# Kernel tuning notes

Measured on AMD Instinct MI355X. Metric: run time of the kernel, lower is better.

Reference implementation:

```python
import jax, jax.numpy as jnp
import numpy as np

B, C, H, W = 64, 2048, 14, 14
D, S, ITERS, EPS, HID = 256, 8, 3, 1e-8, 512


def build_pos(h, w, d):
    gy, gx = np.meshgrid(np.arange(h), np.arange(w), indexing='ij')
    q = d // 4
    omega = 1.0 / (10000.0 ** (np.arange(q) / q))
    ey = gy.reshape(-1, 1) * omega
    ex = gx.reshape(-1, 1) * omega
    pe = np.concatenate([np.sin(ey), np.cos(ey), np.sin(ex), np.cos(ex)], axis=1)
    return jnp.asarray(pe[None], jnp.float32)  # (1, h*w, d)


def layernorm(x, g, b, eps=1e-5):
    m = x.mean(-1, keepdims=True)
    v = ((x - m) ** 2).mean(-1, keepdims=True)
    return (x - m) * jax.lax.rsqrt(v + eps) * g + b


def setup_inputs() -> dict:
    key = jax.random.key(0)
    ks = jax.random.split(key, 16)
    w = lambda k, shp, s=0.02: jax.random.normal(k, shp, jnp.float32) * s
    inp = {
        'x': jax.random.normal(ks[0], (B, C, H, W), jnp.float32),
        'slot_noise': jax.random.normal(ks[1], (B, S, D), jnp.float32),
        'conv_w': w(ks[2], (C, D)), 'conv_b': jnp.zeros((D,), jnp.float32),
        'pos': build_pos(H, W, D),
        'slots_mu': jax.random.normal(ks[3], (1, 1, D), jnp.float32),
        'slots_logsigma': -jnp.ones((1, 1, D), jnp.float32),
        'qw': w(ks[4], (D, D)), 'qb': jnp.zeros((D,), jnp.float32),
        'kw': w(ks[5], (D, D)), 'kb': jnp.zeros((D,), jnp.float32),
        'vw': w(ks[6], (D, D)), 'vb': jnp.zeros((D,), jnp.float32),
        'gru_wih': w(ks[7], (D, 3 * D)), 'gru_whh': w(ks[8], (D, 3 * D)),
        'gru_bih': jnp.zeros((3 * D,), jnp.float32), 'gru_bhh': jnp.zeros((3 * D,), jnp.float32),
        'w1': w(ks[9], (D, HID)), 'b1': jnp.zeros((HID,), jnp.float32),
        'w2': w(ks[10], (HID, D)), 'b2': jnp.zeros((D,), jnp.float32),
        'ln_in_g': jnp.ones((D,), jnp.float32), 'ln_in_b': jnp.zeros((D,), jnp.float32),
        'ln_s_g': jnp.ones((D,), jnp.float32), 'ln_s_b': jnp.zeros((D,), jnp.float32),
        'ln_ff_g': jnp.ones((D,), jnp.float32), 'ln_ff_b': jnp.zeros((D,), jnp.float32),
    }
    return inp


def reference(x, slot_noise, conv_w, conv_b, pos, slots_mu, slots_logsigma,
              qw, qb, kw, kb, vw, vb, gru_wih, gru_whh, gru_bih, gru_bhh,
              w1, b1, w2, b2, ln_in_g, ln_in_b, ln_s_g, ln_s_b, ln_ff_g, ln_ff_b):
    b, c, h, w_ = x.shape
    d = qw.shape[0]
    scale = d ** (-0.5)
    # (B,C,H,W) -> (B,N,C) -> project -> add pos
    xt = x.transpose(0, 2, 3, 1).reshape(b, h * w_, c)
    xt = xt @ conv_w + conv_b + pos
    # slot init
    slots = slots_mu + jnp.exp(slots_logsigma) * slot_noise  # (B,S,D)
    inp = layernorm(xt, ln_in_g, ln_in_b)
    k = inp @ kw + kb
    v = inp @ vw + vb
    attn = None
    for _ in range(ITERS):
        slots_prev = slots
        s = layernorm(slots, ln_s_g, ln_s_b)
        q = s @ qw + qb
        dots = jnp.einsum('bid,bjd->bij', q, k) * scale  # (B,S,N)
        attn = jax.nn.softmax(dots, axis=1) + EPS  # softmax over slots
        attn = attn / attn.sum(-1, keepdims=True)  # renormalize over keys
        updates = jnp.einsum('bjd,bij->bid', v, attn)  # (B,S,D)
        # GRUCell (torch semantics)
        gi = updates @ gru_wih + gru_bih
        gh = slots_prev @ gru_whh + gru_bhh
        ir, iz, inn = jnp.split(gi, 3, axis=-1)
        hr, hz, hn = jnp.split(gh, 3, axis=-1)
        r = jax.nn.sigmoid(ir + hr)
        z = jax.nn.sigmoid(iz + hz)
        nn_ = jnp.tanh(inn + r * hn)
        slots = (1.0 - z) * nn_ + z * slots_prev
        ff = layernorm(slots, ln_ff_g, ln_ff_b)
        slots = slots + (jax.nn.relu(ff @ w1 + b1)) @ w2 + b2
    attn_map = attn.reshape(b, S, h, w_)
    return slots, attn_map
```

## Files before the change

kernel.cpp:

```cpp
#include <hip/hip_runtime.h>
#include <stdint.h>

#define HWN 196
#define CIN 2048
#define DD  256
#define BB  64
#define NSLOT 8
#define KVPAD 224
#define MTOT 12544
#define BKP 128

typedef __attribute__((ext_vector_type(8))) short short8;
typedef __attribute__((ext_vector_type(4))) float f32x4;
typedef __attribute__((ext_vector_type(4))) unsigned short us4;

__device__ __forceinline__ ushort f2bf(float f){ union{float f;uint32_t u;}v;v.f=f;uint32_t u=v.u;return (ushort)((u+0x7FFFu+((u>>16)&1u))>>16);}
__device__ __forceinline__ float bf2f(ushort h){ union{uint32_t u;float f;}v;v.u=((uint32_t)h)<<16;return v.f;}
__device__ __forceinline__ float sigm(float x){ return 1.f/(1.f+expf(-x)); }

__device__ __forceinline__ short8 ldsY(const ushort* buf, int LD, int kt, int lane){
    int row = lane & 15;
    int ch = kt*4 + (lane>>4);
    return *(const short8*)&buf[row*LD + ((ch ^ (row&7))<<3)];
}
// ... 49 lines not shown
        #pragma unroll
        for (int j = 0; j < 8; ++j){ av0[j] = (short)f2bf(areg[j]); av1[j] = (short)f2bf(areg[8+j]); }
        int ch0 = kg*2;
        *(short8*)&As[0][am*BKP + ((ch0^(am&7))<<3)] = av0;
        *(short8*)&As[0][am*BKP + (((ch0+1)^(am&7))<<3)] = av1;
    }
    __syncthreads();
    int cur = 0;
    for (int kt = 0; kt < 8; ++kt){
        if (kt < 7){
            #pragma unroll
            for (int j = 0; j < 16; ++j)
                areg[j] = aptr[(size_t)((kt+1)*BKP + kg*16+j)*HWN];
        }
        short8 bfr[4][2];
        #pragma unroll
        for (int kk = 0; kk < 4; ++kk)
            #pragma unroll
            for (int ni = 0; ni < 2; ++ni){
                int n = wv*32 + ni*16 + (lane&15);
                bfr[kk][ni] = *(const short8*)&cwT[(size_t)n*CIN + kbase + kt*BKP + kk*32 + (lane>>4)*8];
            }
        #pragma unroll
        for (int kk = 0; kk < 4; ++kk){
            short8 afr[4];
            #pragma unroll
            for (int mi = 0; mi < 4; ++mi){
                int row = mi*16 + (lane&15);
                int ch = kk*4 + (lane>>4);
                afr[mi] = *(const short8*)&As[cur][row*BKP + ((ch^(row&7))<<3)];
            }
            #pragma unroll
            for (int mi = 0; mi < 4; ++mi)
                #pragma unroll
                for (int ni = 0; ni < 2; ++ni)
                    acc[mi][ni] = __builtin_amdgcn_mfma_f32_16x16x32_bf16(afr[mi], bfr[kk][ni], acc[mi][ni], 0,0,0);
        }
        if (kt < 7){
            short8 av0, av1;
            #pragma unroll
            for (int j = 0; j < 8; ++j){ av0[j] = (short)f2bf(areg[j]); av1[j] = (short)f2bf(areg[8+j]); }
            int ch0 = kg*2;
            *(short8*)&As[cur^1][am*BKP + ((ch0^(am&7))<<3)] = av0;
            *(short8*)&As[cur^1][am*BKP + (((ch0+1)^(am&7))<<3)] = av1;
        }
        __syncthreads();
        cur ^= 1;
    }
    float* outp = Cpart + (size_t)kq*MTOT*DD;
    #pragma unroll
    for (int mi = 0; mi < 4; ++mi){
        #pragma unroll
        for (int ni = 0; ni < 2; ++ni){
            int n = wv*32 + ni*16 + (lane&15);
            #pragma unroll
            for (int r = 0; r < 4; ++r){
                int m = bm + mi*16 + (lane>>4)*4 + r;
                outp[(size_t)m*DD + n] = acc[mi][ni][r];
            }
        }
    }
}

__global__ __launch_bounds__(512) void k_red(const float* __restrict__ Cpart,
        const float* __restrict__ cb, const float* __restrict__ pos,
        const float* __restrict__ lng, const float* __restrict__ lnb,
        const ushort* __restrict__ kwT, const ushort* __restrict__ vwT,
        const float* __restrict__ kb, const float* __restrict__ vb,
        ushort* __restrict__ kbf, ushort* __restrict__ vT){
    __shared__ ushort As[32*256];
    const int t = threadIdx.x, lane = t & 63, wv = t >> 6;
    const int b = blockIdx.x / 7, pblk = blockIdx.x % 7;
    {
        int row = t >> 4, seg = t & 15;
        int pin = pblk*32 + row;
        int grow = b*HWN + pin;
        if (grow > MTOT-1) grow = MTOT-1;
        int p = pin < HWN ? pin : HWN-1;
        const float* c0 = Cpart + (size_t)grow*DD + seg*16;
        const float* c1 = Cpart + (size_t)MTOT*DD + (size_t)grow*DD + seg*16;
        const float* pp = pos + (size_t)p*DD + seg*16;
        float f[16];
        float s = 0.f, sq = 0.f;
        #pragma unroll
        for (int q = 0; q < 4; ++q){
            f32x4 a  = *(const f32x4*)&c0[q*4];
            f32x4 bq = *(const f32x4*)&c1[q*4];
            f32x4 pv = *(const f32x4*)&pp[q*4];
            f32x4 cv = *(const f32x4*)&cb[seg*16 + q*4];
            #pragma unroll
            for (int r2 = 0; r2 < 4; ++r2){
                float v = a[r2] + bq[r2] + pv[r2] + cv[r2];
                f[q*4+r2] = v; s += v; sq += v*v;
            }
        }
        #pragma unroll
        for (int m = 8; m >= 1; m >>= 1){ s += __shfl_xor(s, m, 64); sq += __shfl_xor(sq, m, 64); }
        float mean = s * (1.f/256.f);
        float rs = rsqrtf(sq*(1.f/256.f) - mean*mean + 1e-5f);
        int d0 = seg*16;
        short8 o0, o1;
        #pragma unroll
        for (int j = 0; j < 8; ++j){
            o0[j] = (short)f2bf((f[j]   - mean)*rs*lng[d0+j]   + lnb[d0+j]);
            o1[j] = (short)f2bf((f[8+j] - mean)*rs*lng[d0+8+j] + lnb[d0+8+j]);
        }
        int ch0 = seg*2;
        *(short8*)&As[row*256 + ((ch0^(row&7))<<3)] = o0;
        *(short8*)&As[row*256 + (((ch0+1)^(row&7))<<3)] = o1;
    }
    __syncthreads();
    f32x4 acck[2][2] = {}, accv[2][2] = {};
    const int n0 = wv*32;
    #pragma unroll
    for (int kt = 0; kt < 8; ++kt){
        short8 afr[2];
        #pragma unroll
        for (int mi = 0; mi < 2; ++mi){
            int row = mi*16 + (lane&15);
            int ch = kt*4 + (lane>>4);
            afr[mi] = *(const short8*)&As[row*256 + ((ch^(row&7))<<3)];
        }
        #pragma unroll
        for (int ni = 0; ni < 2; ++ni){
            int n = n0 + ni*16 + (lane&15);
            int koff = kt*32 + (lane>>4)*8;
            short8 bk = *(const short8*)&kwT[(size_t)n*DD + koff];
            short8 bv = *(const short8*)&vwT[(size_t)n*DD + koff];
            #pragma unroll
            for (int mi = 0; mi < 2; ++mi){
                acck[mi][ni] = __builtin_amdgcn_mfma_f32_16x16x32_bf16(afr[mi], bk, acck[mi][ni],0,0,0);
                accv[mi][ni] = __builtin_amdgcn_mfma_f32_16x16x32_bf16(afr[mi], bv, accv[mi][ni],0,0,0);
            }
        }
    }
    #pragma unroll
    for (int mi = 0; mi < 2; ++mi){
        #pragma unroll
        for (int ni = 0; ni < 2; ++ni){
            int n = n0 + ni*16 + (lane&15);
            float kbn = kb[n], vbn = vb[n];
            int pl0 = pblk*32 + mi*16 + (lane>>4)*4;
            us4 pk;
            #pragma unroll
            for (int r = 0; r < 4; ++r){
                kbf[((size_t)b*KVPAD + pl0 + r)*DD + n] = f2bf(acck[mi][ni][r] + kbn);
                pk[r] = f2bf(accv[mi][ni][r] + vbn);
            }
            *(us4*)&vT[((size_t)b*DD + n)*KVPAD + pl0] = pk;
        }
    }
}

__global__ __launch_bounds__(512) void k_init(const float* __restrict__ noise,
        const float* __restrict__ mu, const float* __restrict__ lsig,
        const ushort* __restrict__ qwT, const float* __restrict__ qb,
        const float* __restrict__ gs, const float* __restrict__ bs,
        float* __restrict__ slots, ushort* __restrict__ qbuf){
    __shared__ float Sld[16*256];
    __shared__ ushort Ysn[16*256];
    __shared__ float part[8][16][2];
    __shared__ float stats[16][2];
    const int t = threadIdx.x, lane = t & 63, w = t >> 6;
    const int bb = blockIdx.x, rbase = bb*16;
    {
        int row = t>>5, ch = t&31; int d = ch*8;
        f32x4 n0 = *(const f32x4*)&noise[(size_t)(rbase+row)*DD + d];
        f32x4 n1 = *(const f32x4*)&noise[(size_t)(rbase+row)*DD + d + 4];
        f32x4 m0 = *(const f32x4*)&mu[d];
        f32x4 m1 = *(const f32x4*)&mu[d+4];
        f32x4 l0 = *(const f32x4*)&lsig[d];
        f32x4 l1 = *(const f32x4*)&lsig[d+4];
        f32x4 s0, s1;
        #pragma unroll
        for (int j = 0; j < 4; ++j){
            s0[j] = m0[j] + expf(l0[j])*n0[j];
            s1[j] = m1[j] + expf(l1[j])*n1[j];
        }
        *(f32x4*)&slots[(size_t)(rbase+row)*DD + d] = s0;
        *(f32x4*)&slots[(size_t)(rbase+row)*DD + d + 4] = s1;
        *(f32x4*)&Sld[row*256 + d] = s0;
        *(f32x4*)&Sld[row*256 + d + 4] = s1;
    }
    __syncthreads();
    f32x4 sv[2];
    #pragma unroll
    for (int sub = 0; sub < 2; ++sub){
        int d0 = w*32 + sub*16 + (lane>>4)*4;
        sv[sub] = *(const f32x4*)&Sld[(lane&15)*256 + d0];
    }
    {
        float lsum = 0.f, lsq = 0.f;
        #pragma unroll
        for (int sub = 0; sub < 2; ++sub)
            #pragma unroll
            for (int r = 0; r < 4; ++r){ float v = sv[sub][r]; lsum += v; lsq += v*v; }
        lsum += __shfl_xor(lsum, 16, 64); lsum += __shfl_xor(lsum, 32, 64);
        lsq  += __shfl_xor(lsq, 16, 64);  lsq  += __shfl_xor(lsq, 32, 64);
        if (lane < 16){ part[w][lane][0] = lsum; part[w][lane][1] = lsq; }
    }
    __syncthreads();
    if (t < 16){
        float a = 0.f, c = 0.f;
        #pragma unroll
        for (int i = 0; i < 8; ++i){ a += part[i][t][0]; c += part[i][t][1]; }
        float mean = a*(1.f/256.f);
        stats[t][0] = mean;
        stats[t][1] = rsqrtf(c*(1.f/256.f) - mean*mean + 1e-5f);
    }
    __syncthreads();
    {
        int slot = lane&15;
        float mean = stats[slot][0], rs = stats[slot][1];
        #pragma unroll
        for (int sub = 0; sub < 2; ++sub){
            int d0 = w*32 + sub*16 + (lane>>4)*4;
            f32x4 g4 = *(const f32x4*)&gs[d0];
            f32x4 b4 = *(const f32x4*)&bs[d0];
            us4 o;
            #pragma unroll
            for (int r = 0; r < 4; ++r) o[r] = f2bf((sv[sub][r]-mean)*rs*g4[r] + b4[r]);
            int ch = d0>>3;
            *(us4*)&Ysn[slot*256 + ((ch^(slot&7))<<3) + (d0&7)] = o;
        }
    }
    __syncthreads();
    f32x4 qa[2] = {};
    #pragma unroll
    for (int kt = 0; kt < 8; ++kt){
        short8 ysn = ldsY(Ysn, 256, kt, lane);
        #pragma unroll
        for (int sub = 0; sub < 2; ++sub){
            int nrow = w*32 + sub*16 + (lane&15);
            short8 xx = gX(qwT, 256, nrow, kt, lane);
            qa[sub] = __builtin_amdgcn_mfma_f32_16x16x32_bf16(xx, ysn, qa[sub], 0,0,0);
        }
    }
    #pragma unroll
    for (int sub = 0; sub < 2; ++sub){
        int qd0 = w*32 + sub*16 + (lane>>4)*4;
        f32x4 qb4 = *(const f32x4*)&qb[qd0];
        us4 o;
        #pragma unroll
        for (int r = 0; r < 4; ++r) o[r] = f2bf((qa[sub][r]+qb4[r])*0.0625f);
        *(us4*)&qbuf[(size_t)(rbase+(lane&15))*DD + qd0] = o;
    }
}

__global__ __launch_bounds__(512) void k_slot(
        const ushort* __restrict__ qbuf, const ushort* __restrict__ kbf,
        const ushort* __restrict__ vT, float* __restrict__ slots,
        ushort* __restrict__ qout,
        const ushort* __restrict__ wihT, const ushort* __restrict__ whhT,
        const float* __restrict__ bih, const float* __restrict__ bhh,
        const ushort* __restrict__ w1T, const float* __restrict__ b1,
        const ushort* __restrict__ w2T, const float* __restrict__ b2,
        const float* __restrict__ gff, const float* __restrict__ bff,
        const float* __restrict__ gs, const float* __restrict__ bs,
        const ushort* __restrict__ qwT, const float* __restrict__ qb,
        float* __restrict__ out_slots, float* __restrict__ out_attn,
        int final_){
    __shared__ ushort Yq[16*256];
    __shared__ ushort Xat[16*256];
    __shared__ ushort Yupd[16*256];
    __shared__ ushort Yslb[16*256];
    __shared__ ushort Ysn[16*256];
    __shared__ ushort Yh[16*512];
    __shared__ float wpart[8][16];
    __shared__ float invk[16];
    __shared__ float part[8][16][2];
    __shared__ float stats[16][2];
    const int t = threadIdx.x, lane = t & 63, w = t >> 6;
    const int b = blockIdx.x;
    const int rbase = b * NSLOT;
    const int srow = lane & 15;
    const int srd = (srow < NSLOT) ? srow : 0;

    if (t < 256){
        int row = t>>5, ch = t&31;
        short8 v = *(const short8*)&qbuf[(size_t)(rbase+row)*DD + ch*8];
        *(short8*)&Yq[row*256 + ((ch^(row&7))<<3)] = v;
        f32x4 s0 = *(const f32x4*)&slots[(size_t)(rbase+row)*DD + ch*8];
        f32x4 s1 = *(const f32x4*)&slots[(size_t)(rbase+row)*DD + ch*8 + 4];
        short8 sv;
        #pragma unroll
        for (int j = 0; j < 4; ++j){ sv[j] = (short)f2bf(s0[j]); sv[4+j] = (short)f2bf(s1[j]); }
        *(short8*)&Yslb[row*256 + ((ch^(row&7))<<3)] = sv;
    } else {
        int i = t - 256;
        int row = (i>>5) + 8, ch = i&31;
        short8 z;
        #pragma unroll
        for (int j = 0; j < 8; ++j) z[j] = 0;
        *(short8*)&Yq[row*256 + ((ch^(row&7))<<3)] = z;
        *(short8*)&Yupd[row*256 + ((ch^(row&7))<<3)] = z;
        *(short8*)&Yslb[row*256 + ((ch^(row&7))<<3)] = z;
    }
    __syncthreads();
    {
        short8 yf[8];
        #pragma unroll
        for (int kt = 0; kt < 8; ++kt) yf[kt] = ldsY(Yq, 256, kt, lane);
        float ps = 0.f;
        #pragma unroll
        for (int rep = 0; rep < 2; ++rep){
            int f = w + rep*8;
            if (f < 14){
                f32x4 acc = {};
                #pragma unroll
                for (int kt = 0; kt < 8; ++kt){
                    short8 xx = gX(kbf + (size_t)b*KVPAD*DD, 256, f*16 + (lane&15), kt, lane);
                    acc = __builtin_amdgcn_mfma_f32_16x16x32_bf16(xx, yf[kt], acc, 0,0,0);
                }
                int k0 = f*16 + (lane>>4)*4;
                us4 o;
                #pragma unroll
                for (int r = 0; r < 4; ++r){
                    float v = acc[r];
                    float mx = v;
                    mx = fmaxf(mx, __shfl_xor(mx, 1, 64));
                    mx = fmaxf(mx, __shfl_xor(mx, 2, 64));
                    mx = fmaxf(mx, __shfl_xor(mx, 4, 64));
                    float e = expf(v - mx);
                    float se = e;
                    se += __shfl_xor(se, 1, 64);
                    se += __shfl_xor(se, 2, 64);
                    se += __shfl_xor(se, 4, 64);
                    float val = e/se + 1e-8f;
                    if (k0 + r >= HWN) val = 0.f;
                    ps += val;
                    o[r] = f2bf(val);
                }
                int ch = k0 >> 3;
                *(us4*)&Xat[srow*256 + ((ch^(srow&7))<<3) + (k0&7)] = o;
            }
        }
        ps += __shfl_xor(ps, 16, 64);
        ps += __shfl_xor(ps, 32, 64);
        if (lane < 16) wpart[w][lane] = ps;
    }
    __syncthreads();
    if (t < 16){
        float s = 0.f;
        #pragma unroll
        for (int i = 0; i < 8; ++i) s += wpart[i][t];
        invk[t] = 1.f/s;
    }
    __syncthreads();
    {
        short8 xa[7];
        #pragma unroll
        for (int kt = 0; kt < 7; ++kt) xa[kt] = ldsY(Xat, 256, kt, lane);
        f32x4 iv = *(const f32x4*)&invk[(lane>>4)*4];
        #pragma unroll
        for (int i = 0; i < 2; ++i){
            int d0 = (w*2 + i)*16;
            f32x4 acc = {};
            #pragma unroll
            for (int kt = 0; kt < 7; ++kt){
                short8 y = gX(vT + (size_t)b*DD*KVPAD, KVPAD, d0 + (lane&15), kt, lane);
                acc = __builtin_amdgcn_mfma_f32_16x16x32_bf16(xa[kt], y, acc, 0,0,0);
            }
            #pragma unroll
            for (int r = 0; r < 4; ++r){
                int s2 = (lane>>4)*4 + r;
                if (s2 < NSLOT){
                    int d = d0 + (lane&15);
                    int ch = d >> 3;
                    Yupd[s2*256 + ((ch^(s2&7))<<3) + (d&7)] = f2bf(acc[r]*iv[r]);
                }
            }
        }
    }
    if (final_){
        for (int idx = t; idx < NSLOT*HWN; idx += 512){
            int slot = idx/HWN, key = idx - slot*HWN;
            int ch = key >> 3;
            out_attn[(size_t)b*NSLOT*HWN + idx] =
                bf2f(Xat[slot*256 + ((ch^(slot&7))<<3) + (key&7)]) * invk[slot];
        }
    }
    __syncthreads();
    f32x4 gi[6] = {}, gh[6] = {};
    #pragma unroll
    for (int kt = 0; kt < 8; ++kt){
        short8 yu = ldsY(Yupd, 256, kt, lane);
        short8 ys = ldsY(Yslb, 256, kt, lane);
        #pragma unroll
        for (int g = 0; g < 3; ++g)
            #pragma unroll
            for (int sub = 0; sub < 2; ++sub){
                int nrow = g*256 + w*32 + sub*16 + (lane&15);
                short8 xi = gX(wihT, 256, nrow, kt, lane);
                short8 xh = gX(whhT, 256, nrow, kt, lane);
                gi[g*2+sub] = __builtin_amdgcn_mfma_f32_16x16x32_bf16(xi, yu, gi[g*2+sub], 0,0,0);
                gh[g*2+sub] = __builtin_amdgcn_mfma_f32_16x16x32_bf16(xh, ys, gh[g*2+sub], 0,0,0);
            }
    }
    f32x4 snew[2];
    #pragma unroll
    for (int sub = 0; sub < 2; ++sub){
        int d0 = w*32 + sub*16 + (lane>>4)*4;
        f32x4 sp  = *(const f32x4*)&slots[(size_t)(rbase + srd)*DD + d0];
        f32x4 bir = *(const f32x4*)&bih[d0];
        f32x4 biz = *(const f32x4*)&bih[256 + d0];
        f32x4 bin = *(const f32x4*)&bih[512 + d0];
        f32x4 bhr = *(const f32x4*)&bhh[d0];
        f32x4 bhz = *(const f32x4*)&bhh[256 + d0];
        f32x4 bhn = *(const f32x4*)&bhh[512 + d0];
        #pragma unroll
        for (int r = 0; r < 4; ++r){
            float ir = gi[0+sub][r] + bir[r];
            float iz = gi[2+sub][r] + biz[r];
            float in_ = gi[4+sub][r] + bin[r];
            float hr = gh[0+sub][r] + bhr[r];
            float hz = gh[2+sub][r] + bhz[r];
            float hn = gh[4+sub][r] + bhn[r];
            float rr = sigm(ir + hr);
            float zz = sigm(iz + hz);
            float nn = tanhf(in_ + rr*hn);
            snew[sub][r] = (1.f - zz)*nn + zz*sp[r];
        }
    }
    {
        float lsum = 0.f, lsq = 0.f;
        #pragma unroll
        for (int sub = 0; sub < 2; ++sub)
            #pragma unroll
            for (int r = 0; r < 4; ++r){ float v = snew[sub][r]; lsum += v; lsq += v*v; }
        lsum += __shfl_xor(lsum, 16, 64); lsum += __shfl_xor(lsum, 32, 64);
        lsq  += __shfl_xor(lsq, 16, 64);  lsq  += __shfl_xor(lsq, 32, 64);
        if (lane < 16){ part[w][lane][0] = lsum; part[w][lane][1] = lsq; }
    }
    __syncthreads();
    if (t < 16){
        float a = 0.f, c = 0.f;
        #pragma unroll
        for (int i = 0; i < 8; ++i){ a += part[i][t][0]; c += part[i][t][1]; }
        float mean = a*(1.f/256.f);
        stats[t][0] = mean;
        stats[t][1] = rsqrtf(c*(1.f/256.f) - mean*mean + 1e-5f);
    }
    __syncthreads();
    {
        float mean = stats[srow][0], rs = stats[srow][1];
        #pragma unroll
        for (int sub = 0; sub < 2; ++sub){
            int d0 = w*32 + sub*16 + (lane>>4)*4;
            f32x4 g4 = *(const f32x4*)&gff[d0];
            f32x4 b4 = *(const f32x4*)&bff[d0];
            us4 o;
            #pragma unroll
            for (int r = 0; r < 4; ++r) o[r] = f2bf((snew[sub][r]-mean)*rs*g4[r] + b4[r]);
            int ch = d0 >> 3;
            *(us4*)&Ysn[srow*256 + ((ch^(srow&7))<<3) + (d0&7)] = o;
        }
    }
    __syncthreads();
    {
        f32x4 hh[4] = {};
        #pragma unroll
        for (int kt = 0; kt < 8; ++kt){
            short8 ysn = ldsY(Ysn, 256, kt, lane);
            #pragma unroll
            for (int s2 = 0; s2 < 4; ++s2){
                int nrow = w*64 + s2*16 + (lane&15);
                short8 xx = gX(w1T, 256, nrow, kt, lane);
                hh[s2] = __builtin_amdgcn_mfma_f32_16x16x32_bf16(xx, ysn, hh[s2], 0,0,0);
            }
        }
        #pragma unroll
        for (int s2 = 0; s2 < 4; ++s2){
            int n0 = w*64 + s2*16 + (lane>>4)*4;
            f32x4 b14 = *(const f32x4*)&b1[n0];
            us4 o;
            #pragma unroll
            for (int r = 0; r < 4; ++r) o[r] = f2bf(fmaxf(hh[s2][r] + b14[r], 0.f));
            int ch = n0 >> 3;
            *(us4*)&Yh[srow*512 + ((ch^(srow&7))<<3) + (n0&7)] = o;
        }
    }
    __syncthreads();
    f32x4 ns[2];
    {
        f32x4 o2[2] = {};
        #pragma unroll
        for (int kt = 0; kt < 16; ++kt){
            short8 yh = ldsY(Yh, 512, kt, lane);
            #pragma unroll
            for (int sub = 0; sub < 2; ++sub){
                int nrow = w*32 + sub*16 + (lane&15);
                short8 xx = gX(w2T, 512, nrow, kt, lane);
                o2[sub] = __builtin_amdgcn_mfma_f32_16x16x32_bf16(xx, yh, o2[sub], 0,0,0);
            }
        }
        float* dst = final_ ? out_slots : slots;
        #pragma unroll
        for (int sub = 0; sub < 2; ++sub){
            int d0 = w*32 + sub*16 + (lane>>4)*4;
            f32x4 b24 = *(const f32x4*)&b2[d0];
            #pragma unroll
            for (int r = 0; r < 4; ++r) ns[sub][r] = o2[sub][r] + b24[r] + snew[sub][r];
            if (srow < NSLOT)
                *(f32x4*)&dst[(size_t)(rbase + srow)*DD + d0] = ns[sub];
        }
    }
    if (final_) return;
    {
        float lsum = 0.f, lsq = 0.f;
        #pragma unroll
        for (int sub = 0; sub < 2; ++sub)
            #pragma unroll
            for (int r = 0; r < 4; ++r){ float v = ns[sub][r]; lsum += v; lsq += v*v; }
        lsum += __shfl_xor(lsum, 16, 64); lsum += __shfl_xor(lsum, 32, 64);
        lsq  += __shfl_xor(lsq, 16, 64);  lsq  += __shfl_xor(lsq, 32, 64);
        if (lane < 16){ part[w][lane][0] = lsum; part[w][lane][1] = lsq; }
    }
    __syncthreads();
    if (t < 16){
        float a = 0.f, c = 0.f;
        #pragma unroll
        for (int i = 0; i < 8; ++i){ a += part[i][t][0]; c += part[i][t][1]; }
        float mean = a*(1.f/256.f);
        stats[t][0] = mean;
        stats[t][1] = rsqrtf(c*(1.f/256.f) - mean*mean + 1e-5f);
    }
    __syncthreads();
    {
        float mean = stats[srow][0], rs = stats[srow][1];
        #pragma unroll
        for (int sub = 0; sub < 2; ++sub){
            int d0 = w*32 + sub*16 + (lane>>4)*4;
            f32x4 g4 = *(const f32x4*)&gs[d0];
            f32x4 b4 = *(const f32x4*)&bs[d0];
            us4 o;
            #pragma unroll
            for (int r = 0; r < 4; ++r) o[r] = f2bf((ns[sub][r]-mean)*rs*g4[r] + b4[r]);
            int ch = d0 >> 3;
            *(us4*)&Ysn[srow*256 + ((ch^(srow&7))<<3) + (d0&7)] = o;
        }
    }
    __syncthreads();
    {
        f32x4 qa[2] = {};
        #pragma unroll
        for (int kt = 0; kt < 8; ++kt){
            short8 ysn = ldsY(Ysn, 256, kt, lane);
            #pragma unroll
            for (int sub = 0; sub < 2; ++sub){
                int nrow = w*32 + sub*16 + (lane&15);
                short8 xx = gX(qwT, 256, nrow, kt, lane);
                qa[sub] = __builtin_amdgcn_mfma_f32_16x16x32_bf16(xx, ysn, qa[sub], 0,0,0);
            }
        }
        #pragma unroll
        for (int sub = 0; sub < 2; ++sub){
            int qd0 = w*32 + sub*16 + (lane>>4)*4;
            f32x4 qb4 = *(const f32x4*)&qb[qd0];
            us4 o;
            #pragma unroll
            for (int r = 0; r < 4; ++r) o[r] = f2bf((qa[sub][r]+qb4[r])*0.0625f);
            if (srow < NSLOT)
                *(us4*)&qout[(size_t)(rbase + srow)*DD + qd0] = o;
        }
    }
}

extern "C" void kernel_launch(void* const* d_in, const int* in_sizes, int n_in,
                              void* d_out, int out_size, void* d_ws, size_t ws_size,
                              hipStream_t stream) {
    const float* x      = (const float*)d_in[0];
    const float* noise  = (const float*)d_in[1];
    const float* conv_w = (const float*)d_in[2];
    const float* conv_b = (const float*)d_in[3];
    const float* pos    = (const float*)d_in[4];
    const float* mu     = (const float*)d_in[5];
    const float* logsig = (const float*)d_in[6];
    const float* qw  = (const float*)d_in[7];
    const float* qb  = (const float*)d_in[8];
    const float* kw  = (const float*)d_in[9];
    const float* kb  = (const float*)d_in[10];
    const float* vw  = (const float*)d_in[11];
    const float* vb  = (const float*)d_in[12];
    const float* wih = (const float*)d_in[13];
    const float* whh = (const float*)d_in[14];
    const float* bih = (const float*)d_in[15];
    const float* bhh = (const float*)d_in[16];
    const float* w1  = (const float*)d_in[17];
    const float* b1  = (const float*)d_in[18];
    const float* w2  = (const float*)d_in[19];
    const float* b2  = (const float*)d_in[20];
    const float* g_in = (const float*)d_in[21];
    const float* b_in = (const float*)d_in[22];
    const float* g_s  = (const float*)d_in[23];
    const float* b_s  = (const float*)d_in[24];
    const float* g_ff = (const float*)d_in[25];
    const float* b_ff = (const float*)d_in[26];

    char* w = (char*)d_ws;
    ushort* kbf    = (ushort*)w; w += (size_t)BB*KVPAD*DD*2;
    ushort* vT     = (ushort*)w; w += (size_t)BB*DD*KVPAD*2;
    ushort* cwT    = (ushort*)w; w += (size_t)DD*CIN*2;
    ushort* qwT    = (ushort*)w; w += (size_t)DD*DD*2;
    ushort* kwT    = (ushort*)w; w += (size_t)DD*DD*2;
    ushort* vwT    = (ushort*)w; w += (size_t)DD*DD*2;
    ushort* wihT   = (ushort*)w; w += (size_t)768*DD*2;
    ushort* whhT   = (ushort*)w; w += (size_t)768*DD*2;
    ushort* w1T    = (ushort*)w; w += (size_t)512*DD*2;
    ushort* w2T    = (ushort*)w; w += (size_t)DD*512*2;
    ushort* qbb    = (ushort*)w; w += (size_t)BB*NSLOT*DD*2;
    float*  slotsb = (float*)w;  w += (size_t)BB*NSLOT*DD*4;
    float*  Cpart  = (float*)w;  w += (size_t)2*MTOT*DD*4;

    float* out_slots = (float*)d_out;
    float* out_attn  = (float*)d_out + (size_t)BB*NSLOT*DD;

    TD8 td;
    td.a[0] = { conv_w, cwT, 2048, 256,    0 };
    td.a[1] = { qw,     qwT,  256, 256,  512 };
    td.a[2] = { kw,     kwT,  256, 256,  576 };
    td.a[3] = { vw,     vwT,  256, 256,  640 };
    td.a[4] = { wih,    wihT, 256, 768,  704 };
    td.a[5] = { whh,    whhT, 256, 768,  896 };
    td.a[6] = { w1,     w1T,  256, 512, 1088 };
    td.a[7] = { w2,     w2T,  512, 256, 1216 };

    k_prep<<<1344, 256, 0, stream>>>(td);
    k_proj<<<392, 512, 0, stream>>>(x, cwT, Cpart);
    k_red<<<448, 512, 0, stream>>>(Cpart, conv_b, pos, g_in, b_in,
                                   kwT, vwT, kb, vb, kbf, vT);
    k_init<<<32, 512, 0, stream>>>(noise, mu, logsig, qwT, qb, g_s, b_s, slotsb, qbb);
    for (int it = 0; it < 3; ++it){
        k_slot<<<BB, 512, 0, stream>>>(qbb, kbf, vT, slotsb, qbb,
                                       wihT, whhT, bih, bhh, w1T, b1, w2T, b2,
                                       g_ff, b_ff, g_s, b_s, qwT, qb,
                                       out_slots, out_attn, it == 2);
    }
}
```

Before: 241.2 us.

## Fuse slot init and all three slot-attention iterations into one kernel

Replaces the k_init kernel and the three k_slot launches with a single kernel, k_iter3. Each block keeps its batch's slots in fp32 in LDS across iterations and computes q into shared memory instead of round-tripping slots and q through global memory. This removes three kernel launches and the global reads and writes of slot and q state between them. It adds extra shared memory for the fp32 slot tile, and the init work is now spread over 64 blocks instead of 32.

```diff
diff --git a/kernel.cpp b/kernel.cpp
--- a/kernel.cpp
+++ b/kernel.cpp
@@ -225,66 +225,32 @@
     }
 }
 
-__global__ __launch_bounds__(512) void k_init(const float* __restrict__ noise,
-        const float* __restrict__ mu, const float* __restrict__ lsig,
+__device__ __forceinline__ void ln_q(const f32x4* ns,
+        const float* __restrict__ gs, const float* __restrict__ bs,
         const ushort* __restrict__ qwT, const float* __restrict__ qb,
-        const float* __restrict__ gs, const float* __restrict__ bs,
-        float* __restrict__ slots, ushort* __restrict__ qbuf){
-    __shared__ float Sld[16*256];
-    __shared__ ushort Ysn[16*256];
-    __shared__ float part[8][16][2];
-    __shared__ float stats[16][2];
-    const int t = threadIdx.x, lane = t & 63, w = t >> 6;
-    const int bb = blockIdx.x, rbase = bb*16;
-    {
-        int row = t>>5, ch = t&31; int d = ch*8;
-        f32x4 n0 = *(const f32x4*)&noise[(size_t)(rbase+row)*DD + d];
-        f32x4 n1 = *(const f32x4*)&noise[(size_t)(rbase+row)*DD + d + 4];
-        f32x4 m0 = *(const f32x4*)&mu[d];
-        f32x4 m1 = *(const f32x4*)&mu[d+4];
-        f32x4 l0 = *(const f32x4*)&lsig[d];
-        f32x4 l1 = *(const f32x4*)&lsig[d+4];
-        f32x4 s0, s1;
-        #pragma unroll
-        for (int j = 0; j < 4; ++j){
-            s0[j] = m0[j] + expf(l0[j])*n0[j];
-            s1[j] = m1[j] + expf(l1[j])*n1[j];
-        }
-        *(f32x4*)&slots[(size_t)(rbase+row)*DD + d] = s0;
-        *(f32x4*)&slots[(size_t)(rbase+row)*DD + d + 4] = s1;
-        *(f32x4*)&Sld[row*256 + d] = s0;
-        *(f32x4*)&Sld[row*256 + d + 4] = s1;
-    }
-    __syncthreads();
-    f32x4 sv[2];
+        ushort* Ysn, ushort* Yq, float* part, float* stats,
+        int w, int lane, int srow){
+    const int t = threadIdx.x;
+    float lsum = 0.f, lsq = 0.f;
     #pragma unroll
-    for (int sub = 0; sub < 2; ++sub){
-        int d0 = w*32 + sub*16 + (lane>>4)*4;
-        sv[sub] = *(const f32x4*)&Sld[(lane&15)*256 + d0];
-    }
-    {
-        float lsum = 0.f, lsq = 0.f;
-        #pragma unroll
-        for (int sub = 0; sub < 2; ++sub)
-            #pragma unroll
-            for (int r = 0; r < 4; ++r){ float v = sv[sub][r]; lsum += v; lsq += v*v; }
-        lsum += __shfl_xor(lsum, 16, 64); lsum += __shfl_xor(lsum, 32, 64);
-        lsq  += __shfl_xor(lsq, 16, 64);  lsq  += __shfl_xor(lsq, 32, 64);
-        if (lane < 16){ part[w][lane][0] = lsum; part[w][lane][1] = lsq; }
-    }
+    for (int sub = 0; sub < 2; ++sub)
+        #pragma unroll
+        for (int r = 0; r < 4; ++r){ float v = ns[sub][r]; lsum += v; lsq += v*v; }
+    lsum += __shfl_xor(lsum, 16, 64); lsum += __shfl_xor(lsum, 32, 64);
+    lsq  += __shfl_xor(lsq, 16, 64);  lsq  += __shfl_xor(lsq, 32, 64);
+    if (lane < 16){ part[(w*16+lane)*2] = lsum; part[(w*16+lane)*2+1] = lsq; }
     __syncthreads();
     if (t < 16){
         float a = 0.f, c = 0.f;
         #pragma unroll
-        for (int i = 0; i < 8; ++i){ a += part[i][t][0]; c += part[i][t][1]; }
+        for (int i = 0; i < 8; ++i){ a += part[(i*16+t)*2]; c += part[(i*16+t)*2+1]; }
         float mean = a*(1.f/256.f);
-        stats[t][0] = mean;
-        stats[t][1] = rsqrtf(c*(1.f/256.f) - mean*mean + 1e-5f);
+        stats[t*2] = mean;
+        stats[t*2+1] = rsqrtf(c*(1.f/256.f) - mean*mean + 1e-5f);
     }
     __syncthreads();
     {
-        int slot = lane&15;
-        float mean = stats[slot][0], rs = stats[slot][1];
+        float mean = stats[srow*2], rs = stats[srow*2+1];
         #pragma unroll
         for (int sub = 0; sub < 2; ++sub){
             int d0 = w*32 + sub*16 + (lane>>4)*4;
@@ -292,57 +258,62 @@
             f32x4 b4 = *(const f32x4*)&bs[d0];
             us4 o;
             #pragma unroll
-            for (int r = 0; r < 4; ++r) o[r] = f2bf((sv[sub][r]-mean)*rs*g4[r] + b4[r]);
-            int ch = d0>>3;
-            *(us4*)&Ysn[slot*256 + ((ch^(slot&7))<<3) + (d0&7)] = o;
+            for (int r = 0; r < 4; ++r) o[r] = f2bf((ns[sub][r]-mean)*rs*g4[r] + b4[r]);
+            int ch = d0 >> 3;
+            *(us4*)&Ysn[srow*256 + ((ch^(srow&7))<<3) + (d0&7)] = o;
         }
     }
     __syncthreads();
-    f32x4 qa[2] = {};
-    #pragma unroll
-    for (int kt = 0; kt < 8; ++kt){
-        short8 ysn = ldsY(Ysn, 256, kt, lane);
+    {
+        f32x4 qa[2] = {};
+        #pragma unroll
+        for (int kt = 0; kt < 8; ++kt){
+            short8 ysn = ldsY(Ysn, 256, kt, lane);
+            #pragma unroll
+            for (int sub = 0; sub < 2; ++sub){
+                int nrow = w*32 + sub*16 + (lane&15);
+                short8 xx = gX(qwT, 256, nrow, kt, lane);
+                qa[sub] = __builtin_amdgcn_mfma_f32_16x16x32_bf16(xx, ysn, qa[sub], 0,0,0);
+            }
+        }
         #pragma unroll
         for (int sub = 0; sub < 2; ++sub){
-            int nrow = w*32 + sub*16 + (lane&15);
-            short8 xx = gX(qwT, 256, nrow, kt, lane);
-            qa[sub] = __builtin_amdgcn_mfma_f32_16x16x32_bf16(xx, ysn, qa[sub], 0,0,0);
-        }
-    }
-    #pragma unroll
-    for (int sub = 0; sub < 2; ++sub){
-        int qd0 = w*32 + sub*16 + (lane>>4)*4;
-        f32x4 qb4 = *(const f32x4*)&qb[qd0];
-        us4 o;
-        #pragma unroll
-        for (int r = 0; r < 4; ++r) o[r] = f2bf((qa[sub][r]+qb4[r])*0.0625f);
-        *(us4*)&qbuf[(size_t)(rbase+(lane&15))*DD + qd0] = o;
-    }
-}
-
-__global__ __launch_bounds__(512) void k_slot(
-        const ushort* __restrict__ qbuf, const ushort* __restrict__ kbf,
-        const ushort* __restrict__ vT, float* __restrict__ slots,
-        ushort* __restrict__ qout,
+            int qd0 = w*32 + sub*16 + (lane>>4)*4;
+            f32x4 qb4 = *(const f32x4*)&qb[qd0];
+            us4 o;
+            #pragma unroll
+            for (int r = 0; r < 4; ++r) o[r] = f2bf((qa[sub][r]+qb4[r])*0.0625f);
+            if (srow < NSLOT){
+                int ch = qd0 >> 3;
+                *(us4*)&Yq[srow*256 + ((ch^(srow&7))<<3) + (qd0&7)] = o;
+            }
+        }
+    }
+}
+
+__global__ __launch_bounds__(512, 1) void k_iter3(
+        const float* __restrict__ noise, const float* __restrict__ mu,
+        const float* __restrict__ lsig,
+        const ushort* __restrict__ qwT, const float* __restrict__ qb,
+        const ushort* __restrict__ kbf, const ushort* __restrict__ vT,
         const ushort* __restrict__ wihT, const ushort* __restrict__ whhT,
         const float* __restrict__ bih, const float* __restrict__ bhh,
         const ushort* __restrict__ w1T, const float* __restrict__ b1,
         const ushort* __restrict__ w2T, const float* __restrict__ b2,
         const float* __restrict__ gff, const float* __restrict__ bff,
         const float* __restrict__ gs, const float* __restrict__ bs,
-        const ushort* __restrict__ qwT, const float* __restrict__ qb,
-        float* __restrict__ out_slots, float* __restrict__ out_attn,
-        int final_){
+        float* __restrict__ out_slots, float* __restrict__ out_attn){
     __shared__ ushort Yq[16*256];
     __shared__ ushort Xat[16*256];
     __shared__ ushort Yupd[16*256];
     __shared__ ushort Yslb[16*256];
     __shared__ ushort Ysn[16*256];
     __shared__ ushort Yh[16*512];
+    __shared__ float Sl[8*256];
     __shared__ float wpart[8][16];
     __shared__ float invk[16];
-    __shared__ float part[8][16][2];
-    __shared__ float stats[16][2];
+    __shared__ float part[8*16*2];
+    __shared__ float stats[16*2];
     const int t = threadIdx.x, lane = t & 63, w = t >> 6;
     const int b = blockIdx.x;
     const int rbase = b * NSLOT;
@@ -350,18 +321,7 @@
     const int srd = (srow < NSLOT) ? srow : 0;
 
     if (t < 256){
-        int row = t>>5, ch = t&31;
-        short8 v = *(const short8*)&qbuf[(size_t)(rbase+row)*DD + ch*8];
-        *(short8*)&Yq[row*256 + ((ch^(row&7))<<3)] = v;
-        f32x4 s0 = *(const f32x4*)&slots[(size_t)(rbase+row)*DD + ch*8];
-        f32x4 s1 = *(const f32x4*)&slots[(size_t)(rbase+row)*DD + ch*8 + 4];
-        short8 sv;
-        #pragma unroll
-        for (int j = 0; j < 4; ++j){ sv[j] = (short)f2bf(s0[j]); sv[4+j] = (short)f2bf(s1[j]); }
-        *(short8*)&Yslb[row*256 + ((ch^(row&7))<<3)] = sv;
-    } else {
-        int i = t - 256;
-        int row = (i>>5) + 8, ch = i&31;
+        int row = (t>>5) + 8, ch = t&31;
         short8 z;
         #pragma unroll
         for (int j = 0; j < 8; ++j) z[j] = 0;
@@ -369,273 +329,245 @@
         *(short8*)&Yupd[row*256 + ((ch^(row&7))<<3)] = z;
         *(short8*)&Yslb[row*256 + ((ch^(row&7))<<3)] = z;
     }
+    {
+        int idx = t*4;
+        int row = idx >> 8, d = idx & 255;
+        f32x4 nz = *(const f32x4*)&noise[((size_t)rbase+row)*DD + d];
+        f32x4 o;
+        #pragma unroll
+        for (int j = 0; j < 4; ++j) o[j] = mu[d+j] + expf(lsig[d+j])*nz[j];
+        *(f32x4*)&Sl[idx] = o;
+    }
     __syncthreads();
-    {
-        short8 yf[8];
-        #pragma unroll
-        for (int kt = 0; kt < 8; ++kt) yf[kt] = ldsY(Yq, 256, kt, lane);
-        float ps = 0.f;
-        #pragma unroll
-        for (int rep = 0; rep < 2; ++rep){
-            int f = w + rep*8;
-            if (f < 14){
-                f32x4 acc = {};
-                #pragma unroll
-                for (int kt = 0; kt < 8; ++kt){
-                    short8 xx = gX(kbf + (size_t)b*KVPAD*DD, 256, f*16 + (lane&15), kt, lane);
-                    acc = __builtin_amdgcn_mfma_f32_16x16x32_bf16(xx, yf[kt], acc, 0,0,0);
-                }
-                int k0 = f*16 + (lane>>4)*4;
-                us4 o;
-                #pragma unroll
-                for (int r = 0; r < 4; ++r){
-                    float v = acc[r];
-                    float mx = v;
-                    mx = fmaxf(mx, __shfl_xor(mx, 1, 64));
-                    mx = fmaxf(mx, __shfl_xor(mx, 2, 64));
-                    mx = fmaxf(mx, __shfl_xor(mx, 4, 64));
-                    float e = expf(v - mx);
-                    float se = e;
-                    se += __shfl_xor(se, 1, 64);
-                    se += __shfl_xor(se, 2, 64);
-                    se += __shfl_xor(se, 4, 64);
-                    float val = e/se + 1e-8f;
-                    if (k0 + r >= HWN) val = 0.f;
-                    ps += val;
-                    o[r] = f2bf(val);
-                }
-                int ch = k0 >> 3;
-                *(us4*)&Xat[srow*256 + ((ch^(srow&7))<<3) + (k0&7)] = o;
-            }
-        }
-        ps += __shfl_xor(ps, 16, 64);
-        ps += __shfl_xor(ps, 32, 64);
-        if (lane < 16) wpart[w][lane] = ps;
-    }
-    __syncthreads();
-    if (t < 16){
-        float s = 0.f;
-        #pragma unroll
-        for (int i = 0; i < 8; ++i) s += wpart[i][t];
-        invk[t] = 1.f/s;
-    }
-    __syncthreads();
-    {
-        short8 xa[7];
-        #pragma unroll
-        for (int kt = 0; kt < 7; ++kt) xa[kt] = ldsY(Xat, 256, kt, lane);
-        f32x4 iv = *(const f32x4*)&invk[(lane>>4)*4];
-        #pragma unroll
-        for (int i = 0; i < 2; ++i){
-            int d0 = (w*2 + i)*16;
-            f32x4 acc = {};
-            #pragma unroll
-            for (int kt = 0; kt < 7; ++kt){
-                short8 y = gX(vT + (size_t)b*DD*KVPAD, KVPAD, d0 + (lane&15), kt, lane);
-                acc = __builtin_amdgcn_mfma_f32_16x16x32_bf16(xa[kt], y, acc, 0,0,0);
-            }
-            #pragma unroll
-            for (int r = 0; r < 4; ++r){
-                int s2 = (lane>>4)*4 + r;
-                if (s2 < NSLOT){
-                    int d = d0 + (lane&15);
-                    int ch = d >> 3;
-                    Yupd[s2*256 + ((ch^(s2&7))<<3) + (d&7)] = f2bf(acc[r]*iv[r]);
-                }
-            }
-        }
-    }
-    if (final_){
-        for (int idx = t; idx < NSLOT*HWN; idx += 512){
-            int slot = idx/HWN, key = idx - slot*HWN;
-            int ch = key >> 3;
-            out_attn[(size_t)b*NSLOT*HWN + idx] =
-                bf2f(Xat[slot*256 + ((ch^(slot&7))<<3) + (key&7)]) * invk[slot];
-        }
-    }
-    __syncthreads();
-    f32x4 gi[6] = {}, gh[6] = {};
-    #pragma unroll
-    for (int kt = 0; kt < 8; ++kt){
-        short8 yu = ldsY(Yupd, 256, kt, lane);
-        short8 ys = ldsY(Yslb, 256, kt, lane);
-        #pragma unroll
-        for (int g = 0; g < 3; ++g)
-            #pragma unroll
-            for (int sub = 0; sub < 2; ++sub){
-                int nrow = g*256 + w*32 + sub*16 + (lane&15);
-                short8 xi = gX(wihT, 256, nrow, kt, lane);
-                short8 xh = gX(whhT, 256, nrow, kt, lane);
-                gi[g*2+sub] = __builtin_amdgcn_mfma_f32_16x16x32_bf16(xi, yu, gi[g*2+sub], 0,0,0);
-                gh[g*2+sub] = __builtin_amdgcn_mfma_f32_16x16x32_bf16(xh, ys, gh[g*2+sub], 0,0,0);
-            }
-    }
-    f32x4 snew[2];
+    f32x4 ns[2];
     #pragma unroll
     for (int sub = 0; sub < 2; ++sub){
         int d0 = w*32 + sub*16 + (lane>>4)*4;
-        f32x4 sp  = *(const f32x4*)&slots[(size_t)(rbase + srd)*DD + d0];
-        f32x4 bir = *(const f32x4*)&bih[d0];
-        f32x4 biz = *(const f32x4*)&bih[256 + d0];
-        f32x4 bin = *(const f32x4*)&bih[512 + d0];
-        f32x4 bhr = *(const f32x4*)&bhh[d0];
-        f32x4 bhz = *(const f32x4*)&bhh[256 + d0];
-        f32x4 bhn = *(const f32x4*)&bhh[512 + d0];
-        #pragma unroll
-        for (int r = 0; r < 4; ++r){
-            float ir = gi[0+sub][r] + bir[r];
-            float iz = gi[2+sub][r] + biz[r];
-            float in_ = gi[4+sub][r] + bin[r];
-            float hr = gh[0+sub][r] + bhr[r];
-            float hz = gh[2+sub][r] + bhz[r];
-            float hn = gh[4+sub][r] + bhn[r];
-            float rr = sigm(ir + hr);
-            float zz = sigm(iz + hz);
-            float nn = tanhf(in_ + rr*hn);
-            snew[sub][r] = (1.f - zz)*nn + zz*sp[r];
-        }
-    }
-    {
-        float lsum = 0.f, lsq = 0.f;
-        #pragma unroll
-        for (int sub = 0; sub < 2; ++sub)
-            #pragma unroll
-            for (int r = 0; r < 4; ++r){ float v = snew[sub][r]; lsum += v; lsq += v*v; }
-        lsum += __shfl_xor(lsum, 16, 64); lsum += __shfl_xor(lsum, 32, 64);
-        lsq  += __shfl_xor(lsq, 16, 64);  lsq  += __shfl_xor(lsq, 32, 64);
-        if (lane < 16){ part[w][lane][0] = lsum; part[w][lane][1] = lsq; }
-    }
-    __syncthreads();
-    if (t < 16){
-        float a = 0.f, c = 0.f;
-        #pragma unroll
-        for (int i = 0; i < 8; ++i){ a += part[i][t][0]; c += part[i][t][1]; }
-        float mean = a*(1.f/256.f);
-        stats[t][0] = mean;
-        stats[t][1] = rsqrtf(c*(1.f/256.f) - mean*mean + 1e-5f);
-    }
-    __syncthreads();
-    {
-        float mean = stats[srow][0], rs = stats[srow][1];
+        ns[sub] = *(const f32x4*)&Sl[srd*256 + d0];
+    }
+    ln_q(ns, gs, bs, qwT, qb, Ysn, Yq, part, stats, w, lane, srow);
+
+    for (int it = 0; it < 3; ++it){
+        if (t < 256){
+            int row = t>>5, ch = t&31;
+            f32x4 s0 = *(const f32x4*)&Sl[row*256 + ch*8];
+            f32x4 s1 = *(const f32x4*)&Sl[row*256 + ch*8 + 4];
+            short8 sv;
+            #pragma unroll
+            for (int j = 0; j < 4; ++j){ sv[j] = (short)f2bf(s0[j]); sv[4+j] = (short)f2bf(s1[j]); }
+            *(short8*)&Yslb[row*256 + ((ch^(row&7))<<3)] = sv;
+        }
+        __syncthreads();
+        {
+            short8 yf[8];
+            #pragma unroll
+            for (int kt = 0; kt < 8; ++kt) yf[kt] = ldsY(Yq, 256, kt, lane);
+            float ps = 0.f;
+            #pragma unroll
+            for (int rep = 0; rep < 2; ++rep){
+                int f = w + rep*8;
+                if (f < 14){
+                    f32x4 acc = {};
+                    #pragma unroll
+                    for (int kt = 0; kt < 8; ++kt){
+                        short8 xx = gX(kbf + (size_t)b*KVPAD*DD, 256, f*16 + (lane&15), kt, lane);
+                        acc = __builtin_amdgcn_mfma_f32_16x16x32_bf16(xx, yf[kt], acc, 0,0,0);
+                    }
+                    int k0 = f*16 + (lane>>4)*4;
+                    us4 o;
+                    #pragma unroll
+                    for (int r = 0; r < 4; ++r){
+                        float v = acc[r];
+                        float mx = v;
+                        mx = fmaxf(mx, __shfl_xor(mx, 1, 64));
+                        mx = fmaxf(mx, __shfl_xor(mx, 2, 64));
+                        mx = fmaxf(mx, __shfl_xor(mx, 4, 64));
+                        float e = expf(v - mx);
+                        float se = e;
+                        se += __shfl_xor(se, 1, 64);
+                        se += __shfl_xor(se, 2, 64);
+                        se += __shfl_xor(se, 4, 64);
+                        float val = e/se + 1e-8f;
+                        if (k0 + r >= HWN) val = 0.f;
+                        ps += val;
+                        o[r] = f2bf(val);
+                    }
+                    int ch = k0 >> 3;
+                    *(us4*)&Xat[srow*256 + ((ch^(srow&7))<<3) + (k0&7)] = o;
+                }
+            }
+            ps += __shfl_xor(ps, 16, 64);
+            ps += __shfl_xor(ps, 32, 64);
+            if (lane < 16) wpart[w][lane] = ps;
+        }
+        __syncthreads();
+        if (t < 16){
+            float s = 0.f;
+            #pragma unroll
+            for (int i = 0; i < 8; ++i) s += wpart[i][t];
+            invk[t] = 1.f/s;
+        }
+        __syncthreads();
+        {
+            short8 xa[7];
+            #pragma unroll
+            for (int kt = 0; kt < 7; ++kt) xa[kt] = ldsY(Xat, 256, kt, lane);
+            f32x4 iv = *(const f32x4*)&invk[(lane>>4)*4];
+            #pragma unroll
+            for (int i = 0; i < 2; ++i){
+                int d0 = (w*2 + i)*16;
+                f32x4 acc = {};
+                #pragma unroll
+                for (int kt = 0; kt < 7; ++kt){
+                    short8 y = gX(vT + (size_t)b*DD*KVPAD, KVPAD, d0 + (lane&15), kt, lane);
+                    acc = __builtin_amdgcn_mfma_f32_16x16x32_bf16(xa[kt], y, acc, 0,0,0);
+                }
+                #pragma unroll
+                for (int r = 0; r < 4; ++r){
+                    int s2 = (lane>>4)*4 + r;
+                    if (s2 < NSLOT){
+                        int d = d0 + (lane&15);
+                        int ch = d >> 3;
+                        Yupd[s2*256 + ((ch^(s2&7))<<3) + (d&7)] = f2bf(acc[r]*iv[r]);
+                    }
+                }
+            }
+        }
+        if (it == 2){
+            for (int idx = t; idx < NSLOT*HWN; idx += 512){
+                int slot = idx/HWN, key = idx - slot*HWN;
+                int ch = key >> 3;
+                out_attn[(size_t)b*NSLOT*HWN + idx] =
+                    bf2f(Xat[slot*256 + ((ch^(slot&7))<<3) + (key&7)]) * invk[slot];
+            }
+        }
+        __syncthreads();
+        f32x4 gi[6] = {}, gh[6] = {};
+        #pragma unroll
+        for (int kt = 0; kt < 8; ++kt){
+            short8 yu = ldsY(Yupd, 256, kt, lane);
+            short8 ys = ldsY(Yslb, 256, kt, lane);
+            #pragma unroll
+            for (int g = 0; g < 3; ++g)
+                #pragma unroll
+                for (int sub = 0; sub < 2; ++sub){
+                    int nrow = g*256 + w*32 + sub*16 + (lane&15);
+                    short8 xi = gX(wihT, 256, nrow, kt, lane);
+                    short8 xh = gX(whhT, 256, nrow, kt, lane);
+                    gi[g*2+sub] = __builtin_amdgcn_mfma_f32_16x16x32_bf16(xi, yu, gi[g*2+sub], 0,0,0);
+                    gh[g*2+sub] = __builtin_amdgcn_mfma_f32_16x16x32_bf16(xh, ys, gh[g*2+sub], 0,0,0);
+                }
+        }
+        f32x4 snew[2];
         #pragma unroll
         for (int sub = 0; sub < 2; ++sub){
             int d0 = w*32 + sub*16 + (lane>>4)*4;
-            f32x4 g4 = *(const f32x4*)&gff[d0];
-            f32x4 b4 = *(const f32x4*)&bff[d0];
-            us4 o;
-            #pragma unroll
-            for (int r = 0; r < 4; ++r) o[r] = f2bf((snew[sub][r]-mean)*rs*g4[r] + b4[r]);
-            int ch = d0 >> 3;
-            *(us4*)&Ysn[srow*256 + ((ch^(srow&7))<<3) + (d0&7)] = o;
-        }
-    }
-    __syncthreads();
-    {
-        f32x4 hh[4] = {};
-        #pragma unroll
-        for (int kt = 0; kt < 8; ++kt){
-            short8 ysn = ldsY(Ysn, 256, kt, lane);
+            f32x4 sp  = *(const f32x4*)&Sl[srd*256 + d0];
+            f32x4 bir = *(const f32x4*)&bih[d0];
+            f32x4 biz = *(const f32x4*)&bih[256 + d0];
+            f32x4 bin = *(const f32x4*)&bih[512 + d0];
+            f32x4 bhr = *(const f32x4*)&bhh[d0];
+            f32x4 bhz = *(const f32x4*)&bhh[256 + d0];
+            f32x4 bhn = *(const f32x4*)&bhh[512 + d0];
+            #pragma unroll
+            for (int r = 0; r < 4; ++r){
+                float ir = gi[0+sub][r] + bir[r];
+                float iz = gi[2+sub][r] + biz[r];
+                float in_ = gi[4+sub][r] + bin[r];
+                float hr = gh[0+sub][r] + bhr[r];
+                float hz = gh[2+sub][r] + bhz[r];
+                float hn = gh[4+sub][r] + bhn[r];
+                float rr = sigm(ir + hr);
+                float zz = sigm(iz + hz);
+                float nn = tanhf(in_ + rr*hn);
+                snew[sub][r] = (1.f - zz)*nn + zz*sp[r];
+            }
+        }
+        {
+            float lsum = 0.f, lsq = 0.f;
+            #pragma unroll
+            for (int sub = 0; sub < 2; ++sub)
+                #pragma unroll
+                for (int r = 0; r < 4; ++r){ float v = snew[sub][r]; lsum += v; lsq += v*v; }
+            lsum += __shfl_xor(lsum, 16, 64); lsum += __shfl_xor(lsum, 32, 64);
+            lsq  += __shfl_xor(lsq, 16, 64);  lsq  += __shfl_xor(lsq, 32, 64);
+            if (lane < 16){ part[(w*16+lane)*2] = lsum; part[(w*16+lane)*2+1] = lsq; }
+        }
+        __syncthreads();
+        if (t < 16){
+            float a = 0.f, c = 0.f;
+            #pragma unroll
+            for (int i = 0; i < 8; ++i){ a += part[(i*16+t)*2]; c += part[(i*16+t)*2+1]; }
+            float mean = a*(1.f/256.f);
+            stats[t*2] = mean;
+            stats[t*2+1] = rsqrtf(c*(1.f/256.f) - mean*mean + 1e-5f);
+        }
+        __syncthreads();
+        {
+            float mean = stats[srow*2], rs = stats[srow*2+1];
+            #pragma unroll
+            for (int sub = 0; sub < 2; ++sub){
+                int d0 = w*32 + sub*16 + (lane>>4)*4;
+                f32x4 g4 = *(const f32x4*)&gff[d0];
+                f32x4 b4 = *(const f32x4*)&bff[d0];
+                us4 o;
+                #pragma unroll
+                for (int r = 0; r < 4; ++r) o[r] = f2bf((snew[sub][r]-mean)*rs*g4[r] + b4[r]);
+                int ch = d0 >> 3;
+                *(us4*)&Ysn[srow*256 + ((ch^(srow&7))<<3) + (d0&7)] = o;
+            }
+        }
+        __syncthreads();
+        {
+            f32x4 hh[4] = {};
+            #pragma unroll
+            for (int kt = 0; kt < 8; ++kt){
+                short8 ysn = ldsY(Ysn, 256, kt, lane);
+                #pragma unroll
+                for (int s2 = 0; s2 < 4; ++s2){
+                    int nrow = w*64 + s2*16 + (lane&15);
+                    short8 xx = gX(w1T, 256, nrow, kt, lane);
+                    hh[s2] = __builtin_amdgcn_mfma_f32_16x16x32_bf16(xx, ysn, hh[s2], 0,0,0);
+                }
+            }
             #pragma unroll
             for (int s2 = 0; s2 < 4; ++s2){
-                int nrow = w*64 + s2*16 + (lane&15);
-                short8 xx = gX(w1T, 256, nrow, kt, lane);
-                hh[s2] = __builtin_amdgcn_mfma_f32_16x16x32_bf16(xx, ysn, hh[s2], 0,0,0);
-            }
-        }
-        #pragma unroll
-        for (int s2 = 0; s2 < 4; ++s2){
-            int n0 = w*64 + s2*16 + (lane>>4)*4;
-            f32x4 b14 = *(const f32x4*)&b1[n0];
-            us4 o;
-            #pragma unroll
-            for (int r = 0; r < 4; ++r) o[r] = f2bf(fmaxf(hh[s2][r] + b14[r], 0.f));
-            int ch = n0 >> 3;
-            *(us4*)&Yh[srow*512 + ((ch^(srow&7))<<3) + (n0&7)] = o;
-        }
-    }
-    __syncthreads();
-    f32x4 ns[2];
-    {
-        f32x4 o2[2] = {};
-        #pragma unroll
-        for (int kt = 0; kt < 16; ++kt){
-            short8 yh = ldsY(Yh, 512, kt, lane);
+                int n0 = w*64 + s2*16 + (lane>>4)*4;
+                f32x4 b14 = *(const f32x4*)&b1[n0];
+                us4 o;
+                #pragma unroll
+                for (int r = 0; r < 4; ++r) o[r] = f2bf(fmaxf(hh[s2][r] + b14[r], 0.f));
+                int ch = n0 >> 3;
+                *(us4*)&Yh[srow*512 + ((ch^(srow&7))<<3) + (n0&7)] = o;
+            }
+        }
+        __syncthreads();
+        {
+            f32x4 o2[2] = {};
+            #pragma unroll
+            for (int kt = 0; kt < 16; ++kt){
+                short8 yh = ldsY(Yh, 512, kt, lane);
+                #pragma unroll
+                for (int sub = 0; sub < 2; ++sub){
+                    int nrow = w*32 + sub*16 + (lane&15);
+                    short8 xx = gX(w2T, 512, nrow, kt, lane);
+                    o2[sub] = __builtin_amdgcn_mfma_f32_16x16x32_bf16(xx, yh, o2[sub], 0,0,0);
+                }
+            }
             #pragma unroll
             for (int sub = 0; sub < 2; ++sub){
-                int nrow = w*32 + sub*16 + (lane&15);
-                short8 xx = gX(w2T, 512, nrow, kt, lane);
-                o2[sub] = __builtin_amdgcn_mfma_f32_16x16x32_bf16(xx, yh, o2[sub], 0,0,0);
-            }
-        }
-        float* dst = final_ ? out_slots : slots;
-        #pragma unroll
-        for (int sub = 0; sub < 2; ++sub){
-            int d0 = w*32 + sub*16 + (lane>>4)*4;
-            f32x4 b24 = *(const f32x4*)&b2[d0];
-            #pragma unroll
-            for (int r = 0; r < 4; ++r) ns[sub][r] = o2[sub][r] + b24[r] + snew[sub][r];
-            if (srow < NSLOT)
-                *(f32x4*)&dst[(size_t)(rbase + srow)*DD + d0] = ns[sub];
-        }
-    }
-    if (final_) return;
-    {
-        float lsum = 0.f, lsq = 0.f;
-        #pragma unroll
-        for (int sub = 0; sub < 2; ++sub)
-            #pragma unroll
-            for (int r = 0; r < 4; ++r){ float v = ns[sub][r]; lsum += v; lsq += v*v; }
-        lsum += __shfl_xor(lsum, 16, 64); lsum += __shfl_xor(lsum, 32, 64);
-        lsq  += __shfl_xor(lsq, 16, 64);  lsq  += __shfl_xor(lsq, 32, 64);
-        if (lane < 16){ part[w][lane][0] = lsum; part[w][lane][1] = lsq; }
-    }
-    __syncthreads();
-    if (t < 16){
-        float a = 0.f, c = 0.f;
-        #pragma unroll
-        for (int i = 0; i < 8; ++i){ a += part[i][t][0]; c += part[i][t][1]; }
-        float mean = a*(1.f/256.f);
-        stats[t][0] = mean;
-        stats[t][1] = rsqrtf(c*(1.f/256.f) - mean*mean + 1e-5f);
-    }
-    __syncthreads();
-    {
-        float mean = stats[srow][0], rs = stats[srow][1];
-        #pragma unroll
-        for (int sub = 0; sub < 2; ++sub){
-            int d0 = w*32 + sub*16 + (lane>>4)*4;
-            f32x4 g4 = *(const f32x4*)&gs[d0];
-            f32x4 b4 = *(const f32x4*)&bs[d0];
-            us4 o;
-            #pragma unroll
-            for (int r = 0; r < 4; ++r) o[r] = f2bf((ns[sub][r]-mean)*rs*g4[r] + b4[r]);
-            int ch = d0 >> 3;
-            *(us4*)&Ysn[srow*256 + ((ch^(srow&7))<<3) + (d0&7)] = o;
-        }
-    }
-    __syncthreads();
-    {
-        f32x4 qa[2] = {};
-        #pragma unroll
-        for (int kt = 0; kt < 8; ++kt){
-            short8 ysn = ldsY(Ysn, 256, kt, lane);
-            #pragma unroll
-            for (int sub = 0; sub < 2; ++sub){
-                int nrow = w*32 + sub*16 + (lane&15);
-                short8 xx = gX(qwT, 256, nrow, kt, lane);
-                qa[sub] = __builtin_amdgcn_mfma_f32_16x16x32_bf16(xx, ysn, qa[sub], 0,0,0);
-            }
-        }
-        #pragma unroll
-        for (int sub = 0; sub < 2; ++sub){
-            int qd0 = w*32 + sub*16 + (lane>>4)*4;
-            f32x4 qb4 = *(const f32x4*)&qb[qd0];
-            us4 o;
-            #pragma unroll
-            for (int r = 0; r < 4; ++r) o[r] = f2bf((qa[sub][r]+qb4[r])*0.0625f);
-            if (srow < NSLOT)
-                *(us4*)&qout[(size_t)(rbase + srow)*DD + qd0] = o;
-        }
+                int d0 = w*32 + sub*16 + (lane>>4)*4;
+                f32x4 b24 = *(const f32x4*)&b2[d0];
+                #pragma unroll
+                for (int r = 0; r < 4; ++r) ns[sub][r] = o2[sub][r] + b24[r] + snew[sub][r];
+                if (srow < NSLOT){
+                    if (it == 2) *(f32x4*)&out_slots[((size_t)rbase + srow)*DD + d0] = ns[sub];
+                    else         *(f32x4*)&Sl[srow*256 + d0] = ns[sub];
+                }
+            }
+        }
+        if (it < 2)
+            ln_q(ns, gs, bs, qwT, qb, Ysn, Yq, part, stats, w, lane, srow);
     }
 }
 
@@ -681,8 +613,6 @@
     ushort* whhT   = (ushort*)w; w += (size_t)768*DD*2;
     ushort* w1T    = (ushort*)w; w += (size_t)512*DD*2;
     ushort* w2T    = (ushort*)w; w += (size_t)DD*512*2;
-    ushort* qbb    = (ushort*)w; w += (size_t)BB*NSLOT*DD*2;
-    float*  slotsb = (float*)w;  w += (size_t)BB*NSLOT*DD*4;
     float*  Cpart  = (float*)w;  w += (size_t)2*MTOT*DD*4;
 
     float* out_slots = (float*)d_out;
@@ -702,11 +632,7 @@
     k_proj<<<392, 512, 0, stream>>>(x, cwT, Cpart);
     k_red<<<448, 512, 0, stream>>>(Cpart, conv_b, pos, g_in, b_in,
                                    kwT, vwT, kb, vb, kbf, vT);
-    k_init<<<32, 512, 0, stream>>>(noise, mu, logsig, qwT, qb, g_s, b_s, slotsb, qbb);
-    for (int it = 0; it < 3; ++it){
-        k_slot<<<BB, 512, 0, stream>>>(qbb, kbf, vT, slotsb, qbb,
-                                       wihT, whhT, bih, bhh, w1T, b1, w2T, b2,
-                                       g_ff, b_ff, g_s, b_s, qwT, qb,
-                                       out_slots, out_attn, it == 2);
-    }
-}
+    k_iter3<<<BB, 512, 0, stream>>>(noise, mu, logsig, qwT, qb, kbf, vT,
+                                    wihT, whhT, bih, bhh, w1T, b1, w2T, b2,
+                                    g_ff, b_ff, g_s, b_s, out_slots, out_attn);
+}
```

After: 373.9 us. 1.55x slower.
